# Kernel optimization log

Measured on AMD Instinct MI355X. Metric: run time of the kernel, lower is better.

Reference implementation:

```python
import jax, jax.numpy as jnp
import numpy as np

DIM = 512
HEADS = 8
HEAD_DIM = DIM // HEADS
SCALE = HEAD_DIM ** -0.5
EPS = 1e-5


def setup_inputs() -> dict:
    key = jax.random.key(0)
    ks = jax.random.split(key, 6)
    B, N, C = 4, 2048, DIM
    x = jax.random.normal(ks[0], (B, N, C), dtype=jnp.float32)
    w_qkv = jax.random.normal(ks[1], (C, 3 * C), dtype=jnp.float32) * (C ** -0.5)
    w_proj = jax.random.normal(ks[2], (C, C), dtype=jnp.float32) * (C ** -0.5)
    b_proj = jax.random.normal(ks[3], (C,), dtype=jnp.float32) * 0.02
    gamma = jnp.ones((C,), dtype=jnp.float32)
    beta = jnp.zeros((C,), dtype=jnp.float32)
    return {"x": x, "w_qkv": w_qkv, "w_proj": w_proj, "b_proj": b_proj,
            "gamma": gamma, "beta": beta}


def reference(x, w_qkv, w_proj, b_proj, gamma, beta):
    B, N, C = x.shape
    # LayerNorm over channel dim
    mu = jnp.mean(x, axis=-1, keepdims=True)
    var = jnp.mean(jnp.square(x - mu), axis=-1, keepdims=True)
    xn = (x - mu) * jax.lax.rsqrt(var + EPS) * gamma + beta
    # QKV projection (fp32, no bias)
    qkv = xn @ w_qkv  # [B, N, 3C]
    qkv = qkv.reshape(B, N, 3, HEADS, HEAD_DIM)
    q = jnp.transpose(qkv[:, :, 0], (0, 2, 1, 3))  # [B, H, N, D]
    k = jnp.transpose(qkv[:, :, 1], (0, 2, 1, 3))
    v = jnp.transpose(qkv[:, :, 2], (0, 2, 1, 3))
    attn = jnp.einsum('bhnd,bhmd->bhnm', q, k) * SCALE
    attn = jax.nn.softmax(attn, axis=-1)
    out = jnp.einsum('bhnm,bhmd->bhnd', attn, v)  # [B, H, N, D]
    out = jnp.transpose(out, (0, 2, 1, 3)).reshape(B, N, C)
    out = out @ w_proj + b_proj
    return x + out
```

## Files before the change

### kernel.cpp

```cpp
#include <hip/hip_runtime.h>
#include <hip/hip_bf16.h>
#include <math.h>

typedef _Float16 f16;
typedef _Float16 half8 __attribute__((ext_vector_type(8)));
typedef _Float16 half4 __attribute__((ext_vector_type(4)));
typedef float f32x4 __attribute__((ext_vector_type(4)));
typedef unsigned int uint;
typedef unsigned int u32x4 __attribute__((ext_vector_type(4)));

#define DIMC 512
#define HEADS 8
#define HD 64
#define BB 4
#define NN 2048
#define MM (BB*NN)
#define NQKV (3*DIMC)
#define SCALE 0.125f
#define LOG2E 1.44269504f
#define EPSLN 1e-5f

__device__ __forceinline__ void g2l16(const void* g, void* l) {
    __builtin_amdgcn_global_load_lds(
        (const __attribute__((address_space(1))) unsigned int*)g,
        (__attribute__((address_space(3))) unsigned int*)l, 16, 0, 0);
}

__device__ __forceinline__ void ln_rows(const float* __restrict__ x,
                                        const float* __restrict__ gamma,
                                        const float* __restrict__ beta,
                                        f16* __restrict__ xn, int blk) {
    int w = threadIdx.x >> 6;
    int lane = threadIdx.x & 63;
    int row = blk * 4 + w;
    const float* xr = x + (size_t)row * DIMC;
    float4 v0 = ((const float4*)xr)[lane * 2];
    float4 v1 = ((const float4*)xr)[lane * 2 + 1];
    float s = v0.x + v0.y + v0.z + v0.w + v1.x + v1.y + v1.z + v1.w;
#pragma unroll
    for (int off = 1; off < 64; off <<= 1) s += __shfl_xor(s, off);
    float mu = s * (1.0f / DIMC);
    float d0 = v0.x - mu, d1 = v0.y - mu, d2 = v0.z - mu, d3 = v0.w - mu;
    float d4 = v1.x - mu, d5 = v1.y - mu, d6 = v1.z - mu, d7 = v1.w - mu;
    float s2 = d0*d0 + d1*d1 + d2*d2 + d3*d3 + d4*d4 + d5*d5 + d6*d6 + d7*d7;
#pragma unroll
    for (int off = 1; off < 64; off <<= 1) s2 += __shfl_xor(s2, off);
    float rstd = rsqrtf(s2 * (1.0f / DIMC) + EPSLN);
    float4 g0 = ((const float4*)gamma)[lane * 2];
    float4 g1 = ((const float4*)gamma)[lane * 2 + 1];
    float4 b0 = ((const float4*)beta)[lane * 2];
    float4 b1 = ((const float4*)beta)[lane * 2 + 1];
    half8 o;
    o[0] = (f16)(d0 * rstd * g0.x + b0.x);
    o[1] = (f16)(d1 * rstd * g0.y + b0.y);
    o[2] = (f16)(d2 * rstd * g0.z + b0.z);
    o[3] = (f16)(d3 * rstd * g0.w + b0.w);
    o[4] = (f16)(d4 * rstd * g1.x + b1.x);
    o[5] = (f16)(d5 * rstd * g1.y + b1.y);
    o[6] = (f16)(d6 * rstd * g1.z + b1.z);
    o[7] = (f16)(d7 * rstd * g1.w + b1.w);
    ((half8*)(xn + (size_t)row * DIMC))[lane] = o;
}

__device__ __forceinline__ void transp_tile(const float* __restrict__ src,
                                            f16* __restrict__ dst,
                                            int R, int C, int k0, int n0) {
    __shared__ f16 t[32][72];
    int tid = threadIdx.x;
    int rr = tid >> 6, col = tid & 63;
#pragma unroll
    for (int p = 0; p < 8; p++) {
        int r = p * 4 + rr;
        t[r][col] = (f16)src[(size_t)(k0 + r) * C + n0 + col];
    }
    __syncthreads();
    int nl = tid >> 2, kc = (tid & 3) * 8;
    half8 v;
#pragma unroll
    for (int j = 0; j < 8; j++) v[j] = t[kc + j][nl];
    *(half8*)&dst[(size_t)(n0 + nl) * R + k0 + kc] = v;
}

__global__ __launch_bounds__(256) void prep_kernel(const float* __restrict__ x,
                                                   const float* __restrict__ gamma,
                                                   const float* __restrict__ beta,
                                                   const float* __restrict__ wqkv,
                                                   const float* __restrict__ wproj,
                                                   f16* __restrict__ xn,
                                                   f16* __restrict__ wqkvt,
                                                   f16* __restrict__ wprojt) {
    int bid = blockIdx.x;
    if (bid < 2048) {
        ln_rows(x, gamma, beta, xn, bid);
    } else if (bid < 2048 + 384) {
        int b2 = bid - 2048;
        int bx = b2 % 24, by = b2 / 24;
        transp_tile(wqkv, wqkvt, DIMC, NQKV, by * 32, bx * 64);
    } else {
        int b2 = bid - 2048 - 384;
        int bx = b2 % 8, by = b2 / 8;
        transp_tile(wproj, wprojt, DIMC, DIMC, by * 32, bx * 64);
    }
}

__device__ __forceinline__ void gemm128_loop(const char* Ag, const char* Bg,
                                             f16* As, f16* Bs, f32x4 (&acc)[4][4]) {
    int tid = threadIdx.x;
    int w = tid >> 6, lane = tid & 63, l15 = lane & 15, quad = lane >> 4;
    int wy = w >> 1, wx = w & 1;
    int off0 = w * 1024 + lane * 16;
#define QSTAGE(kk, b) do { \
    _Pragma("unroll") \
    for (int c = 0; c < 2; ++c) { \
        int off = c * 4096 + off0; \
        int row = off >> 6, col = off & 63; \
        g2l16(Ag + (size_t)row * 1024 + (kk) * 64 + col, (char*)As + (b) * 8192 + c * 4096 + w * 1024); \
        g2l16(Bg + (size_t)row * 1024 + (kk) * 64 + col, (char*)Bs + (b) * 8192 + c * 4096 + w * 1024); \
    } } while (0)
    QSTAGE(0, 0);
    __syncthreads();
    for (int kk = 0; kk < 16; ++kk) {
        int cb = kk & 1;
        if (kk < 15) QSTAGE(kk + 1, cb ^ 1);
        half8 af[4], bf[4];
#pragma unroll
        for (int i = 0; i < 4; ++i) {
            af[i] = *(const half8*)((const char*)As + cb * 8192 + ((wy * 64 + i * 16 + l15) << 6) + quad * 16);
            bf[i] = *(const half8*)((const char*)Bs + cb * 8192 + ((wx * 64 + i * 16 + l15) << 6) + quad * 16);
        }
#pragma unroll
        for (int i = 0; i < 4; ++i)
#pragma unroll
            for (int j = 0; j < 4; ++j)
                acc[i][j] = __builtin_amdgcn_mfma_f32_16x16x32_f16(af[i], bf[j], acc[i][j], 0, 0, 0);
        __syncthreads();
    }
#undef QSTAGE
}

__global__ __launch_bounds__(256) void gemm_qkv(const f16* __restrict__ xn,
                                                const f16* __restrict__ wt,
                                                f16* __restrict__ qb,
                                                f16* __restrict__ kbuf,
                                                f16* __restrict__ vtb) {
    __shared__ __align__(16) f16 As[2 * 128 * 32];
    __shared__ __align__(16) f16 Bs[2 * 128 * 32];
    int tid = threadIdx.x;
    int w = tid >> 6, lane = tid & 63, l15 = lane & 15, quad = lane >> 4;
    int wy = w >> 1, wx = w & 1;
    int m0 = blockIdx.y * 128, c0 = blockIdx.x * 128;
    f32x4 acc[4][4] = {};
    gemm128_loop((const char*)(xn + (size_t)m0 * DIMC),
                 (const char*)(wt + (size_t)c0 * DIMC), As, Bs, acc);
    int bx = blockIdx.x;
    if (bx < 8) {
        const float QS = SCALE * LOG2E;
        f16* dst = (bx < 4) ? qb : kbuf;
        float mul = (bx < 4) ? QS : 1.0f;
        int cb = (bx < 4) ? c0 : c0 - DIMC;
#pragma unroll
        for (int i = 0; i < 4; ++i)
#pragma unroll
            for (int j = 0; j < 4; ++j)
#pragma unroll
                for (int r = 0; r < 4; ++r) {
                    int m = m0 + wy * 64 + i * 16 + quad * 4 + r;
                    int c = cb + wx * 64 + j * 16 + l15;
                    int b = m >> 11, n = m & 2047;
                    int h = c >> 6, d = c & 63;
                    dst[(((size_t)(b * HEADS + h)) * NN + n) * HD + d] = (f16)(acc[i][j][r] * mul);
                }
    } else {
        __syncthreads();
        f16* T = (f16*)As + w * 512;
        int cb = c0 - 2 * DIMC;
        int dl = lane >> 2, mp = lane & 3;
#pragma unroll
        for (int i = 0; i < 4; ++i)
#pragma unroll
            for (int j = 0; j < 4; ++j) {
                half4 hv;
#pragma unroll
                for (int r = 0; r < 4; ++r) hv[r] = (f16)acc[i][j][r];
                *(half4*)&T[l15 * 20 + quad * 4] = hv;
                half4 rv = *(half4*)&T[dl * 20 + mp * 4];
                int c = cb + wx * 64 + j * 16 + dl;
                int m = m0 + wy * 64 + i * 16 + mp * 4;
                int b = m >> 11, n = m & 2047;
                int h = c >> 6, d = c & 63;
                *(half4*)&vtb[(((size_t)(b * HEADS + h)) * HD + d) * NN + n] = rv;
            }
    }
}

__global__ __launch_bounds__(256, 4) void attn_kernel(const f16* __restrict__ qb,
                                                      const f16* __restrict__ kbuf,
                                                      const f16* __restrict__ vtb,
                                                      f16* __restrict__ ao) {
    __shared__ __align__(16) f16 KV[16384];
    int id = blockIdx.x;
    int xcd = id & 7, slot = id >> 3;
    int bh = xcd * 4 + (slot >> 4);
    int qt4 = slot & 15;
    int n0 = qt4 * 128;
    int tid = threadIdx.x, w = tid >> 6, lane = tid & 63, l15 = lane & 15, quad = lane >> 4;
    const f16* Kbase = kbuf + (size_t)bh * NN * HD;
    const f16* Vbase = vtb + (size_t)bh * HD * NN;
    const f16* Qbase = qb + (size_t)bh * NN * HD;
    half8 qf[2][2];
#pragma unroll
    for (int qt = 0; qt < 2; ++qt) {
        const f16* qr = Qbase + (size_t)(n0 + w * 32 + qt * 16 + l15) * HD + quad * 8;
        qf[qt][0] = *(const half8*)qr;
        qf[qt][1] = *(const half8*)(qr + 32);
    }
    f32x4 ot[2][4] = {};
    f32x4 lacc[2] = {};
    half8 ones8;
#pragma unroll
    for (int j = 0; j < 8; ++j) ones8[j] = (f16)1.0f;
    int rx = (l15 & 7) << 4;
    int lrow = lane >> 3;
    int scolb = ((lane & 7) << 4) ^ (lrow << 4);
    int rbase = w * 16;
    {
        char* K0 = (char*)KV;
        char* V0 = (char*)KV + 8192;
#pragma unroll
        for (int c = 0; c < 2; ++c) {
            int r0 = rbase + c * 8;
            g2l16((const char*)Kbase + (size_t)(r0 + lrow) * (HD * 2) + scolb,
                  K0 + r0 * 128);
            g2l16((const char*)Vbase + (size_t)(r0 + lrow) * (NN * 2) + scolb,
                  V0 + r0 * 128);
        }
    }
    __syncthreads();
    for (int it = 0; it < NN / 64; ++it) {
        int cur = it & 1;
        char* Kc = (char*)KV + (cur << 14);
        char* Vc = Kc + 8192;
        if (it < NN / 64 - 1) {
            char* Kn = (char*)KV + ((cur ^ 1) << 14);
            char* Vn = Kn + 8192;
            int k0 = (it + 1) * 64;
#pragma unroll
            for (int c = 0; c < 2; ++c) {
                int r0 = rbase + c * 8;
                g2l16((const char*)Kbase + (size_t)(k0 + r0 + lrow) * (HD * 2) + scolb,
                      Kn + r0 * 128);
                g2l16((const char*)Vbase + (size_t)(r0 + lrow) * (NN * 2) + k0 * 2 + scolb,
                      Vn + r0 * 128);
            }
        }
        f32x4 s0[4], s1[4];
        __builtin_amdgcn_s_setprio(1);
#pragma unroll
        for (int kt = 0; kt < 4; ++kt) {
            int rb = (kt * 16 + l15) * 128;
            half8 a0 = *(const half8*)(Kc + rb + ((quad * 16) ^ rx));
            half8 a1 = *(const half8*)(Kc + rb + ((64 + quad * 16) ^ rx));
            f32x4 z0 = {};
            z0 = __builtin_amdgcn_mfma_f32_16x16x32_f16(a0, qf[0][0], z0, 0, 0, 0);
            z0 = __builtin_amdgcn_mfma_f32_16x16x32_f16(a1, qf[0][1], z0, 0, 0, 0);
            s0[kt] = z0;
            f32x4 z1 = {};
            z1 = __builtin_amdgcn_mfma_f32_16x16x32_f16(a0, qf[1][0], z1, 0, 0, 0);
            z1 = __builtin_amdgcn_mfma_f32_16x16x32_f16(a1, qf[1][1], z1, 0, 0, 0);
            s1[kt] = z1;
        }
        __builtin_amdgcn_s_setprio(0);
        uint up[2][4][2];
#pragma unroll
        for (int kt = 0; kt < 4; ++kt) {
            up[0][kt][0] = __builtin_bit_cast(uint, __builtin_amdgcn_cvt_pkrtz(
                __builtin_amdgcn_exp2f(s0[kt][0]), __builtin_amdgcn_exp2f(s0[kt][1])));
            up[0][kt][1] = __builtin_bit_cast(uint, __builtin_amdgcn_cvt_pkrtz(
                __builtin_amdgcn_exp2f(s0[kt][2]), __builtin_amdgcn_exp2f(s0[kt][3])));
            up[1][kt][0] = __builtin_bit_cast(uint, __builtin_amdgcn_cvt_pkrtz(
                __builtin_amdgcn_exp2f(s1[kt][0]), __builtin_amdgcn_exp2f(s1[kt][1])));
            up[1][kt][1] = __builtin_bit_cast(uint, __builtin_amdgcn_cvt_pkrtz(
                __builtin_amdgcn_exp2f(s1[kt][2]), __builtin_amdgcn_exp2f(s1[kt][3])));
        }
        __builtin_amdgcn_s_setprio(1);
#pragma unroll
        for (int kc = 0; kc < 2; ++kc) {
            int cb = (kc * 64 + quad * 16) ^ rx;
            half8 av[4];
#pragma unroll
            for (int dt = 0; dt < 4; ++dt)
                av[dt] = *(const half8*)(Vc + (dt * 16 + l15) * 128 + cb);
#pragma unroll
            for (int qt = 0; qt < 2; ++qt) {
                u32x4 pw;
#pragma unroll
                for (int i = 0; i < 2; ++i) {
                    uint x = up[qt][kc * 2][i], y = up[qt][kc * 2 + 1][i];
                    asm volatile("v_permlane32_swap_b32 %0, %1" : "+v"(x), "+v"(y));
                    asm volatile("v_permlane16_swap_b32 %0, %1" : "+v"(x), "+v"(y));
                    pw[i] = x; pw[2 + i] = y;
                }
                half8 pb8 = __builtin_bit_cast(half8, pw);
                lacc[qt] = __builtin_amdgcn_mfma_f32_16x16x32_f16(ones8, pb8, lacc[qt], 0, 0, 0);
#pragma unroll
                for (int dt = 0; dt < 4; ++dt)
                    ot[qt][dt] = __builtin_amdgcn_mfma_f32_16x16x32_f16(av[dt], pb8, ot[qt][dt], 0, 0, 0);
            }
        }
        __builtin_amdgcn_s_setprio(0);
        __syncthreads();
    }
    float inv[2] = { 1.0f / lacc[0][0], 1.0f / lacc[1][0] };
    char* Tc = (char*)KV + w * 4096;
#pragma unroll
    for (int qt = 0; qt < 2; ++qt)
#pragma unroll
        for (int dt = 0; dt < 4; ++dt) {
            half4 hv;
#pragma unroll
            for (int r = 0; r < 4; ++r) hv[r] = (f16)(ot[qt][dt][r] * inv[qt]);
            *(half4*)(Tc + (qt * 16 + l15) * 128 + ((dt * 32 + quad * 8) ^ rx)) = hv;
        }
    __syncthreads();
    int b = bh >> 3, h = bh & 7;
#pragma unroll
    for (int j = 0; j < 4; ++j) {
        int nl = j * 8 + (lane >> 3);
        int d16 = (lane & 7) * 16;
        half8 v = *(const half8*)(Tc + nl * 128 + (d16 ^ ((nl & 7) << 4)));
        int n = n0 + w * 32 + nl;
        *(half8*)&ao[((size_t)(b * NN + n)) * DIMC + h * HD + (lane & 7) * 8] = v;
    }
}

__global__ __launch_bounds__(256) void gemm_proj(const f16* __restrict__ aob,
                                                 const f16* __restrict__ wt,
                                                 const float* __restrict__ x,
                                                 const float* __restrict__ bias,
                                                 float* __restrict__ out) {
    __shared__ __align__(16) f16 As[2 * 128 * 32];
    __shared__ __align__(16) f16 Bs[2 * 64 * 32];
    int tid = threadIdx.x;
    int w = tid >> 6, lane = tid & 63, l15 = lane & 15, quad = lane >> 4;
    int m0 = blockIdx.y * 128, c0 = blockIdx.x * 64;
    const char* Ag = (const char*)(aob + (size_t)m0 * DIMC);
    const char* Bg = (const char*)(wt + (size_t)c0 * DIMC);
    f32x4 acc[2][4] = {};
    int off0 = w * 1024 + lane * 16;
#define PSTAGE(kk, b) do { \
    _Pragma("unroll") \
    for (int c = 0; c < 2; ++c) { \
        int off = c * 4096 + off0; \
        int row = off >> 6, col = off & 63; \
        g2l16(Ag + (size_t)row * 1024 + (kk) * 64 + col, (char*)As + (b) * 8192 + c * 4096 + w * 1024); \
    } \
    { \
        int off = tid * 16; \
        int row = off >> 6, col = off & 63; \
        g2l16(Bg + (size_t)row * 1024 + (kk) * 64 + col, (char*)Bs + (b) * 4096 + w * 1024); \
    } } while (0)
    PSTAGE(0, 0);
    __syncthreads();
    for (int kk = 0; kk < 16; ++kk) {
        int cb = kk & 1;
        if (kk < 15) PSTAGE(kk + 1, cb ^ 1);
        half8 af[2], bf[4];
#pragma unroll
        for (int i = 0; i < 2; ++i)
            af[i] = *(const half8*)((const char*)As + cb * 8192 + ((w * 32 + i * 16 + l15) << 6) + quad * 16);
#pragma unroll
        for (int j = 0; j < 4; ++j)
            bf[j] = *(const half8*)((const char*)Bs + cb * 4096 + ((j * 16 + l15) << 6) + quad * 16);
#pragma unroll
        for (int i = 0; i < 2; ++i)
#pragma unroll
            for (int j = 0; j < 4; ++j)
                acc[i][j] = __builtin_amdgcn_mfma_f32_16x16x32_f16(af[i], bf[j], acc[i][j], 0, 0, 0);
        __syncthreads();
    }
#undef PSTAGE
#pragma unroll
    for (int i = 0; i < 2; ++i)
#pragma unroll
        for (int j = 0; j < 4; ++j)
#pragma unroll
            for (int r = 0; r < 4; ++r) {
                int m = m0 + w * 32 + i * 16 + quad * 4 + r;
                int c = c0 + j * 16 + l15;
                out[(size_t)m * DIMC + c] = x[(size_t)m * DIMC + c] + bias[c] + acc[i][j][r];
            }
}

extern "C" void kernel_launch(void* const* d_in, const int* in_sizes, int n_in,
                              void* d_out, int out_size, void* d_ws, size_t ws_size,
                              hipStream_t stream) {
    (void)in_sizes; (void)n_in; (void)out_size; (void)ws_size;
    const float* x     = (const float*)d_in[0];
    const float* wqkv  = (const float*)d_in[1];
    const float* wproj = (const float*)d_in[2];
    const float* bproj = (const float*)d_in[3];
    const float* gamma = (const float*)d_in[4];
    const float* beta  = (const float*)d_in[5];
    float* out = (float*)d_out;

    char* ws = (char*)d_ws;
    f16* xn     = (f16*)ws;                 ws += (size_t)MM * DIMC * 2;
    f16* wqkvt  = (f16*)ws;                 ws += (size_t)NQKV * DIMC * 2;
    f16* wprojt = (f16*)ws;                 ws += (size_t)DIMC * DIMC * 2;
    f16* qbuf   = (f16*)ws;                 ws += (size_t)MM * DIMC * 2;
    f16* kbuf   = (f16*)ws;                 ws += (size_t)MM * DIMC * 2;
    f16* vtbuf  = (f16*)ws;                 ws += (size_t)MM * DIMC * 2;
    f16* aobuf  = (f16*)ws;                 ws += (size_t)MM * DIMC * 2;

    prep_kernel<<<2048 + 384 + 128, 256, 0, stream>>>(x, gamma, beta, wqkv, wproj,
                                                      xn, wqkvt, wprojt);
    gemm_qkv<<<dim3(NQKV / 128, MM / 128), 256, 0, stream>>>(xn, wqkvt, qbuf, kbuf, vtbuf);
    attn_kernel<<<NN / 128 * BB * HEADS, 256, 0, stream>>>(qbuf, kbuf, vtbuf, aobuf);
    gemm_proj<<<dim3(DIMC / 64, MM / 128), 256, 0, stream>>>(aobuf, wprojt, x, bproj, out);
}
```

Measured before the change: 157.0 us.

## Split attention KV range across two wave groups per block with LDS reduction

Doubles the attention block to 512 threads, with two wave groups each handling half of the key/value sequence for the same 128 query rows. Partial outputs and row sums from the second group are reduced into the first group through shared memory before normalization and store. This raises the waves available per query tile so the small grid fills the CUs better. In exchange it doubles the LDS footprint, adds a reduction and extra barriers, and may tighten register limits.

```diff
diff --git a/kernel.cpp b/kernel.cpp
--- a/kernel.cpp
+++ b/kernel.cpp
@@ -193,24 +193,25 @@
     }
 }
 
-__global__ __launch_bounds__(256, 4) void attn_kernel(const f16* __restrict__ qb,
+__global__ __launch_bounds__(512, 4) void attn_kernel(const f16* __restrict__ qb,
                                                       const f16* __restrict__ kbuf,
                                                       const f16* __restrict__ vtb,
                                                       f16* __restrict__ ao) {
-    __shared__ __align__(16) f16 KV[16384];
+    __shared__ __align__(16) f16 KV[32768];
     int id = blockIdx.x;
     int xcd = id & 7, slot = id >> 3;
     int bh = xcd * 4 + (slot >> 4);
     int qt4 = slot & 15;
     int n0 = qt4 * 128;
     int tid = threadIdx.x, w = tid >> 6, lane = tid & 63, l15 = lane & 15, quad = lane >> 4;
+    int g = w >> 2, wq = w & 3;
     const f16* Kbase = kbuf + (size_t)bh * NN * HD;
     const f16* Vbase = vtb + (size_t)bh * HD * NN;
     const f16* Qbase = qb + (size_t)bh * NN * HD;
     half8 qf[2][2];
 #pragma unroll
     for (int qt = 0; qt < 2; ++qt) {
-        const f16* qr = Qbase + (size_t)(n0 + w * 32 + qt * 16 + l15) * HD + quad * 8;
+        const f16* qr = Qbase + (size_t)(n0 + wq * 32 + qt * 16 + l15) * HD + quad * 8;
         qf[qt][0] = *(const half8*)qr;
         qf[qt][1] = *(const half8*)(qr + 32);
     }
@@ -222,37 +223,23 @@
     int rx = (l15 & 7) << 4;
     int lrow = lane >> 3;
     int scolb = ((lane & 7) << 4) ^ (lrow << 4);
-    int rbase = w * 16;
-    {
-        char* K0 = (char*)KV;
-        char* V0 = (char*)KV + 8192;
-#pragma unroll
-        for (int c = 0; c < 2; ++c) {
-            int r0 = rbase + c * 8;
-            g2l16((const char*)Kbase + (size_t)(r0 + lrow) * (HD * 2) + scolb,
-                  K0 + r0 * 128);
-            g2l16((const char*)Vbase + (size_t)(r0 + lrow) * (NN * 2) + scolb,
-                  V0 + r0 * 128);
-        }
-    }
-    __syncthreads();
-    for (int it = 0; it < NN / 64; ++it) {
+#define ASTAGE(it_, dstb) do { \
+    _Pragma("unroll") \
+    for (int c = 0; c < 2; ++c) { \
+        int base = w * 16 + c * 8; \
+        int grp = base >> 6, loc = base & 63; \
+        g2l16((const char*)Kbase + (size_t)(grp * 1024 + (it_) * 64 + loc + lrow) * (HD * 2) + scolb, \
+              (char*)KV + (dstb) + grp * 8192 + loc * 128); \
+        g2l16((const char*)Vbase + (size_t)(loc + lrow) * (NN * 2) + (size_t)(grp * 1024 + (it_) * 64) * 2 + scolb, \
+              (char*)KV + (dstb) + 16384 + grp * 8192 + loc * 128); \
+    } } while (0)
+    ASTAGE(0, 0);
+    __syncthreads();
+    for (int it = 0; it < NN / 128; ++it) {
         int cur = it & 1;
-        char* Kc = (char*)KV + (cur << 14);
-        char* Vc = Kc + 8192;
-        if (it < NN / 64 - 1) {
-            char* Kn = (char*)KV + ((cur ^ 1) << 14);
-            char* Vn = Kn + 8192;
-            int k0 = (it + 1) * 64;
-#pragma unroll
-            for (int c = 0; c < 2; ++c) {
-                int r0 = rbase + c * 8;
-                g2l16((const char*)Kbase + (size_t)(k0 + r0 + lrow) * (HD * 2) + scolb,
-                      Kn + r0 * 128);
-                g2l16((const char*)Vbase + (size_t)(r0 + lrow) * (NN * 2) + k0 * 2 + scolb,
-                      Vn + r0 * 128);
-            }
-        }
+        char* Kc = (char*)KV + (cur << 15) + g * 8192;
+        char* Vc = (char*)KV + (cur << 15) + 16384 + g * 8192;
+        if (it < NN / 128 - 1) ASTAGE(it + 1, (cur ^ 1) << 15);
         f32x4 s0[4], s1[4];
         __builtin_amdgcn_s_setprio(1);
 #pragma unroll
@@ -310,26 +297,58 @@
         __builtin_amdgcn_s_setprio(0);
         __syncthreads();
     }
-    float inv[2] = { 1.0f / lacc[0][0], 1.0f / lacc[1][0] };
-    char* Tc = (char*)KV + w * 4096;
-#pragma unroll
-    for (int qt = 0; qt < 2; ++qt)
-#pragma unroll
-        for (int dt = 0; dt < 4; ++dt) {
-            half4 hv;
-#pragma unroll
-            for (int r = 0; r < 4; ++r) hv[r] = (f16)(ot[qt][dt][r] * inv[qt]);
-            *(half4*)(Tc + (qt * 16 + l15) * 128 + ((dt * 32 + quad * 8) ^ rx)) = hv;
+#undef ASTAGE
+    float l0 = lacc[0][0], l1 = lacc[1][0];
+    int lsw = (lane & 7) << 4;
+    if (w >= 4) {
+        char* dst = (char*)KV + (w - 4) * 8192 + lane * 128;
+#pragma unroll
+        for (int qt = 0; qt < 2; ++qt)
+#pragma unroll
+            for (int dt = 0; dt < 4; ++dt)
+                *(f32x4*)(dst + (((qt * 4 + dt) * 16) ^ lsw)) = ot[qt][dt];
+        float2 lv; lv.x = l0; lv.y = l1;
+        *(float2*)((char*)KV + 49152 + ((w - 4) * 64 + lane) * 8) = lv;
+    }
+    __syncthreads();
+    if (w < 4) {
+        char* src = (char*)KV + w * 8192 + lane * 128;
+#pragma unroll
+        for (int qt = 0; qt < 2; ++qt)
+#pragma unroll
+            for (int dt = 0; dt < 4; ++dt) {
+                f32x4 p = *(const f32x4*)(src + (((qt * 4 + dt) * 16) ^ lsw));
+                ot[qt][dt] += p;
+            }
+        float2 lv = *(const float2*)((char*)KV + 49152 + (w * 64 + lane) * 8);
+        l0 += lv.x; l1 += lv.y;
+    }
+    __syncthreads();
+    if (w < 4) {
+        float inv[2] = { 1.0f / l0, 1.0f / l1 };
+        char* Tc = (char*)KV + 32768 + w * 4096;
+#pragma unroll
+        for (int qt = 0; qt < 2; ++qt)
+#pragma unroll
+            for (int dt = 0; dt < 4; ++dt) {
+                half4 hv;
+#pragma unroll
+                for (int r = 0; r < 4; ++r) hv[r] = (f16)(ot[qt][dt][r] * inv[qt]);
+                *(half4*)(Tc + (qt * 16 + l15) * 128 + ((dt * 32 + quad * 8) ^ rx)) = hv;
+            }
+    }
+    __syncthreads();
+    if (w < 4) {
+        char* Tc = (char*)KV + 32768 + w * 4096;
+        int b = bh >> 3, h = bh & 7;
+#pragma unroll
+        for (int j = 0; j < 4; ++j) {
+            int nl = j * 8 + (lane >> 3);
+            int d16 = (lane & 7) * 16;
+            half8 v = *(const half8*)(Tc + nl * 128 + (d16 ^ ((nl & 7) << 4)));
+            int n = n0 + w * 32 + nl;
+            *(half8*)&ao[((size_t)(b * NN + n)) * DIMC + h * HD + (lane & 7) * 8] = v;
         }
-    __syncthreads();
-    int b = bh >> 3, h = bh & 7;
-#pragma unroll
-    for (int j = 0; j < 4; ++j) {
-        int nl = j * 8 + (lane >> 3);
-        int d16 = (lane & 7) * 16;
-        half8 v = *(const half8*)(Tc + nl * 128 + (d16 ^ ((nl & 7) << 4)));
-        int n = n0 + w * 32 + nl;
-        *(half8*)&ao[((size_t)(b * NN + n)) * DIMC + h * HD + (lane & 7) * 8] = v;
     }
 }
 
@@ -415,6 +434,6 @@
     prep_kernel<<<2048 + 384 + 128, 256, 0, stream>>>(x, gamma, beta, wqkv, wproj,
                                                       xn, wqkvt, wprojt);
     gemm_qkv<<<dim3(NQKV / 128, MM / 128), 256, 0, stream>>>(xn, wqkvt, qbuf, kbuf, vtbuf);
-    attn_kernel<<<NN / 128 * BB * HEADS, 256, 0, stream>>>(qbuf, kbuf, vtbuf, aobuf);
+    attn_kernel<<<NN / 128 * BB * HEADS, 512, 0, stream>>>(qbuf, kbuf, vtbuf, aobuf);
     gemm_proj<<<dim3(DIMC / 64, MM / 128), 256, 0, stream>>>(aobuf, wprojt, x, bproj, out);
 }
```

New measurement: 157.6 us. About the same (+0.4%).
